# Kernel tuning notes

Hardware: AMD Instinct MI355X
Metric: run time of the kernel (lower is better)

The kernel has to match this reference:

```python
import jax, jax.numpy as jnp
import numpy as np

B, L, H, D = 2, 2048, 16, 64


def setup_inputs() -> dict:
    key = jax.random.key(0)
    k1, k2, k3, k4 = jax.random.split(key, 4)
    query_states = jax.random.normal(k1, (B, L, H, D), dtype=jnp.float32)
    key_states = jax.random.normal(k2, (B, L, H, D), dtype=jnp.float32)
    # per-head linear feature maps (LinearFeatureMap parameters)
    Wq = jax.random.normal(k3, (H, D, D), dtype=jnp.float32)
    Wk = jax.random.normal(k4, (H, D, D), dtype=jnp.float32)
    return {"query_states": query_states, "key_states": key_states, "Wq": Wq, "Wk": Wk}


def reference(query_states, key_states, Wq, Wk):
    # per-head linear feature map: [B,L,H,D] x [H,D,E] -> [B,L,H,E]
    q = jnp.einsum('blhd,hde->blhe', query_states, Wq)
    k = jnp.einsum('blhd,hde->blhe', key_states, Wk)
    # kernelized attention scores: [B,H,L,S]
    attn = jnp.einsum('blhd,bshd->bhls', q, k)
    # sum-normalization over keys (non-softmax normalizer)
    attn = attn / jnp.sum(attn, axis=-1, keepdims=True)
    return attn
```

## Files before the change

kernel.cpp:

```cpp
#include <hip/hip_runtime.h>
#include <stdint.h>

#define NB 2
#define NL 2048
#define NH 16
#define ND 64

typedef __attribute__((ext_vector_type(8))) short short8;
typedef __attribute__((ext_vector_type(4))) float f32x4;
typedef __attribute__((ext_vector_type(4))) unsigned short ushort4v;

__device__ __forceinline__ unsigned short f2bf_rne(float x) {
    union { float f; unsigned int u; } v; v.f = x;
    unsigned int r = v.u + 0x7fffu + ((v.u >> 16) & 1u);
    return (unsigned short)(r >> 16);
}
__device__ __forceinline__ float bf2f(unsigned short b) {
    union { unsigned int u; float f; } v; v.u = ((unsigned int)b) << 16;
    return v.f;
}

__global__ __launch_bounds__(256) void proj_bf16_kernel(const float* __restrict__ x,
                                                        const float* __restrict__ W,
                                                        unsigned short* __restrict__ ph,
                                                        unsigned short* __restrict__ pl) {
    __shared__ float Wlds[ND * ND];
    __shared__ float xs[128 * 68];
    const int blk = blockIdx.x;
    const int lc = blk & 15;
    const int h = (blk >> 4) & 15;
    const int b = blk >> 8;
    const int l0 = lc * 128;
    const int t = threadIdx.x;

    {
        const float4* src = (const float4*)(W + (size_t)h * ND * ND);
#pragma unroll
        for (int i = 0; i < 4; ++i)
            ((float4*)Wlds)[t + 256 * i] = src[t + 256 * i];
    }
    {
#pragma unroll
        for (int i = 0; i < 8; ++i) {
            const int idx = t + 256 * i;
            const int r = idx >> 4, c = idx & 15;
            const float4 v = *(const float4*)(x + (((size_t)b * NL + l0 + r) * NH + h) * ND + c * 4);
            *(float4*)&xs[r * 68 + c * 4] = v;
        }
    }
    __syncthreads();

    const int e4 = (t & 15) * 4;
    const int rg = t >> 4;
    float acc[8][4] = {};
    for (int d = 0; d < ND; ++d) {
        const float4 w4 = *(const float4*)&Wlds[d * ND + e4];
#pragma unroll
        for (int it = 0; it < 8; ++it) {
            const float xv = xs[(rg + it * 16) * 68 + d];
            acc[it][0] += xv * w4.x; acc[it][1] += xv * w4.y;
            acc[it][2] += xv * w4.z; acc[it][3] += xv * w4.w;
        }
    }

    unsigned short* phh = ph + ((size_t)(b * NH + h) * NL + l0) * ND;
    unsigned short* pll = pl + ((size_t)(b * NH + h) * NL + l0) * ND;
#pragma unroll
    for (int it = 0; it < 8; ++it) {
        const int r = rg + it * 16;
        const int ep = e4 ^ ((r & 7) << 3);
        ushort4v hv, lv;
#pragma unroll
        for (int j = 0; j < 4; ++j) {
            const unsigned short hb = f2bf_rne(acc[it][j]);
            hv[j] = hb;
            lv[j] = f2bf_rne(acc[it][j] - bf2f(hb));
        }
        *(ushort4v*)&phh[(size_t)r * ND + ep] = hv;
        *(ushort4v*)&pll[(size_t)r * ND + ep] = lv;
    }
}

__global__ __launch_bounds__(1024) void xsum_kernel(const float* __restrict__ key,
                                                    double* __restrict__ xsumk) {
    __shared__ double part[16][64];
    const int bh = blockIdx.x;
    const int b = bh >> 4, h = bh & 15;
    const int t = threadIdx.x;
    const int e = t & 63, c = t >> 6;
    const float* base = key + ((size_t)b * NL * NH + h) * ND + e;
    double acc = 0.0;
    for (int s = c * 128; s < (c + 1) * 128; ++s)
        acc += (double)base[(size_t)s * (NH * ND)];
    part[c][e] = acc;
    __syncthreads();
    if (t < 64) {
        double s2 = 0.0;
#pragma unroll
        for (int c2 = 0; c2 < 16; ++c2) s2 += part[c2][e];
        xsumk[(size_t)bh * ND + e] = s2;
    }
}

__global__ __launch_bounds__(64) void prep_kernel(const double* __restrict__ xsumk,
                                                  const float* __restrict__ Wq,
                                                  const float* __restrict__ Wk,
                                                  double* __restrict__ v) {
    __shared__ double xs[ND], ks[ND];
    const int bh = blockIdx.x;
    const int h = bh & 15;
    const int t = threadIdx.x;
    xs[t] = xsumk[(size_t)bh * ND + t];
    __syncthreads();
    {
        double acc = 0.0;
        const float* wk = Wk + (size_t)h * ND * ND + t;
        for (int d = 0; d < ND; ++d) acc += xs[d] * (double)wk[(size_t)d * ND];
        ks[t] = acc;
    }
    __syncthreads();
    {
        double acc = 0.0;
        const float* wq = Wq + (size_t)h * ND * ND + (size_t)t * ND;
        for (int e = 0; e < ND; ++e) acc += (double)wq[e] * ks[e];
        v[(size_t)bh * ND + t] = acc;
    }
}

__global__ __launch_bounds__(256) void den_kernel(const float* __restrict__ xq,
                                                  const double* __restrict__ v,
                                                  float* __restrict__ invden) {
    __shared__ double vs[ND];
    const int bh = blockIdx.x;
    const int b = bh >> 4, h = bh & 15;
    const int t = threadIdx.x;
    if (t < 64) vs[t] = v[(size_t)bh * ND + t];
    __syncthreads();
    const int l = blockIdx.y * 256 + t;
    const float* xp = xq + (((size_t)b * NL + l) * NH + h) * ND;
    double acc = 0.0;
#pragma unroll 8
    for (int d = 0; d < ND; ++d) acc += (double)xp[d] * vs[d];
    invden[(size_t)bh * NL + l] = (float)(1.0 / acc);
}

__global__ __launch_bounds__(256) void attn_kernel(const unsigned short* __restrict__ qbh,
                                                   const unsigned short* __restrict__ qbl,
                                                   const unsigned short* __restrict__ kbh,
                                                   const unsigned short* __restrict__ kbl,
                                                   const float* __restrict__ invden,
                                                   float* __restrict__ out) {
    __shared__ unsigned short smem[4 * 128 * 64];
    const int bh = blockIdx.z;
    const int l0 = blockIdx.y * 128, s0 = blockIdx.x * 128;
    const int t = threadIdx.x;
    const int w = t >> 6, ln = t & 63;

    {
        const size_t pan = (size_t)bh * NL * ND;
        const unsigned short* srcs[4] = {qbh + pan + (size_t)l0 * ND,
                                         qbl + pan + (size_t)l0 * ND,
                                         kbh + pan + (size_t)s0 * ND,
                                         kbl + pan + (size_t)s0 * ND};
#pragma unroll
        for (int arr = 0; arr < 4; ++arr) {
            const unsigned short* s = srcs[arr] + w * 2048 + ln * 8;
            unsigned short* d = smem + arr * 8192 + w * 2048;
#pragma unroll
            for (int u = 0; u < 4; ++u) {
                __builtin_amdgcn_global_load_lds((const __attribute__((address_space(1))) unsigned int*)(s + u * 512),
                                                 (__attribute__((address_space(3))) unsigned int*)(d + u * 512),
                                                 16, 0, 0);
            }
        }
    }
    __syncthreads();

    const int wr = w >> 1, wc = w & 1;
    const int fr = ln & 15, g = ln >> 4;
    const int swz = (fr & 7) << 4;

    f32x4 acc[4][4];
#pragma unroll
    for (int i = 0; i < 4; ++i)
#pragma unroll
        for (int j = 0; j < 4; ++j) acc[i][j] = (f32x4){0.f, 0.f, 0.f, 0.f};

    const char* sb = (const char*)smem;
#pragma unroll
    for (int kc = 0; kc < 2; ++kc) {
        const int cofs = ((kc << 6) | (g << 4)) ^ swz;
        short8 kh_f[4], kl_f[4], qh_f[4], ql_f[4];
#pragma unroll
        for (int i = 0; i < 4; ++i) {
            const int arow = wr * 64 + i * 16 + fr;
            kh_f[i] = *(const short8*)(sb + 2 * 16384 + arow * 128 + cofs);
            kl_f[i] = *(const short8*)(sb + 3 * 16384 + arow * 128 + cofs);
            const int brow = wc * 64 + i * 16 + fr;
            qh_f[i] = *(const short8*)(sb + 0 * 16384 + brow * 128 + cofs);
            ql_f[i] = *(const short8*)(sb + 1 * 16384 + brow * 128 + cofs);
        }
#pragma unroll
        for (int i = 0; i < 4; ++i)
#pragma unroll
            for (int j = 0; j < 4; ++j) {
                acc[i][j] = __builtin_amdgcn_mfma_f32_16x16x32_bf16(kh_f[i], qh_f[j], acc[i][j], 0, 0, 0);
                acc[i][j] = __builtin_amdgcn_mfma_f32_16x16x32_bf16(kh_f[i], ql_f[j], acc[i][j], 0, 0, 0);
                acc[i][j] = __builtin_amdgcn_mfma_f32_16x16x32_bf16(kl_f[i], qh_f[j], acc[i][j], 0, 0, 0);
            }
    }

    const float* invp = invden + (size_t)bh * NL + l0 + wc * 64 + fr;
#pragma unroll
    for (int j = 0; j < 4; ++j) {
        const float inv = invp[j * 16];
        float* orow = out + ((size_t)bh * NL + l0 + wc * 64 + j * 16 + fr) * NL + s0 + wr * 64 + g * 4;
#pragma unroll
        for (int i = 0; i < 4; ++i) {
            const f32x4 a = acc[i][j];
            float4 vv;
            vv.x = a[0] * inv; vv.y = a[1] * inv; vv.z = a[2] * inv; vv.w = a[3] * inv;
            *(float4*)(orow + i * 16) = vv;
        }
    }
}

extern "C" void kernel_launch(void* const* d_in, const int* in_sizes, int n_in,
                              void* d_out, int out_size, void* d_ws, size_t ws_size,
                              hipStream_t stream) {
    const float* query = (const float*)d_in[0];
    const float* key   = (const float*)d_in[1];
    const float* Wq    = (const float*)d_in[2];
    const float* Wk    = (const float*)d_in[3];
    float* out = (float*)d_out;

    const size_t npan = (size_t)NB * NH * NL * ND;
    char* ws = (char*)d_ws;
    unsigned short* qbh = (unsigned short*)(ws);
    unsigned short* qbl = (unsigned short*)(ws + 1 * npan * 2);
    unsigned short* kbh = (unsigned short*)(ws + 2 * npan * 2);
    unsigned short* kbl = (unsigned short*)(ws + 3 * npan * 2);
    double* xsumk = (double*)(ws + 4 * npan * 2);
    double* v     = (double*)(ws + 4 * npan * 2 + 16384);
    float* invden = (float*)(ws + 4 * npan * 2 + 32768);

    proj_bf16_kernel<<<NB * NH * (NL / 128), 256, 0, stream>>>(query, Wq, qbh, qbl);
    proj_bf16_kernel<<<NB * NH * (NL / 128), 256, 0, stream>>>(key, Wk, kbh, kbl);
    xsum_kernel<<<NB * NH, 1024, 0, stream>>>(key, xsumk);
    prep_kernel<<<NB * NH, 64, 0, stream>>>(xsumk, Wq, Wk, v);
    den_kernel<<<dim3(NB * NH, NL / 256), 256, 0, stream>>>(query, v, invden);
    attn_kernel<<<dim3(NL / 128, NL / 128, NB * NH), 256, 0, stream>>>(qbh, qbl, kbh, kbl, invden, out);
}
```

Measured before the change: 193.1 us.

## Load MFMA fragments directly from global memory and remap blocks across XCDs

The attention kernel stops staging Q/K bf16 hi/lo tiles in LDS and instead loads each short8 fragment straight from global memory, which removes the LDS swizzle and the block barrier. The projection kernel writes unswizzled layouts to match. The grid is flattened to 1D and block IDs are remapped so that consecutive tiles of the same head land on the same XCD for L2 reuse. Output stores become nontemporal to avoid polluting the cache with the large write-once result. Direct global fragment loads may be less coalesced and rely on L2 hits in exchange for zero LDS traffic.

```diff
diff --git a/kernel.cpp b/kernel.cpp
--- a/kernel.cpp
+++ b/kernel.cpp
@@ -68,7 +68,6 @@
 #pragma unroll
     for (int it = 0; it < 8; ++it) {
         const int r = rg + it * 16;
-        const int ep = e4 ^ ((r & 7) << 3);
         ushort4v hv, lv;
 #pragma unroll
         for (int j = 0; j < 4; ++j) {
@@ -76,8 +75,8 @@
             hv[j] = hb;
             lv[j] = f2bf_rne(acc[it][j] - bf2f(hb));
         }
-        *(ushort4v*)&phh[(size_t)r * ND + ep] = hv;
-        *(ushort4v*)&pll[(size_t)r * ND + ep] = lv;
+        *(ushort4v*)&phh[(size_t)r * ND + e4] = hv;
+        *(ushort4v*)&pll[(size_t)r * ND + e4] = lv;
     }
 }
 
@@ -150,35 +149,21 @@
                                                    const unsigned short* __restrict__ kbl,
                                                    const float* __restrict__ invden,
                                                    float* __restrict__ out) {
-    __shared__ unsigned short smem[4 * 128 * 64];
-    const int bh = blockIdx.z;
-    const int l0 = blockIdx.y * 128, s0 = blockIdx.x * 128;
+    const int orig = blockIdx.x;
+    const int wid = (orig & 7) * 1024 + (orig >> 3);
+    const int st = wid & 15, lt = (wid >> 4) & 15, bh = wid >> 8;
+    const int l0 = lt * 128, s0 = st * 128;
+
     const int t = threadIdx.x;
     const int w = t >> 6, ln = t & 63;
-
-    {
-        const size_t pan = (size_t)bh * NL * ND;
-        const unsigned short* srcs[4] = {qbh + pan + (size_t)l0 * ND,
-                                         qbl + pan + (size_t)l0 * ND,
-                                         kbh + pan + (size_t)s0 * ND,
-                                         kbl + pan + (size_t)s0 * ND};
-#pragma unroll
-        for (int arr = 0; arr < 4; ++arr) {
-            const unsigned short* s = srcs[arr] + w * 2048 + ln * 8;
-            unsigned short* d = smem + arr * 8192 + w * 2048;
-#pragma unroll
-            for (int u = 0; u < 4; ++u) {
-                __builtin_amdgcn_global_load_lds((const __attribute__((address_space(1))) unsigned int*)(s + u * 512),
-                                                 (__attribute__((address_space(3))) unsigned int*)(d + u * 512),
-                                                 16, 0, 0);
-            }
-        }
-    }
-    __syncthreads();
-
     const int wr = w >> 1, wc = w & 1;
     const int fr = ln & 15, g = ln >> 4;
-    const int swz = (fr & 7) << 4;
+
+    const size_t pan = (size_t)bh * NL * ND;
+    const unsigned short* qh_p = qbh + pan;
+    const unsigned short* ql_p = qbl + pan;
+    const unsigned short* kh_p = kbh + pan;
+    const unsigned short* kl_p = kbl + pan;
 
     f32x4 acc[4][4];
 #pragma unroll
@@ -186,19 +171,18 @@
 #pragma unroll
         for (int j = 0; j < 4; ++j) acc[i][j] = (f32x4){0.f, 0.f, 0.f, 0.f};
 
-    const char* sb = (const char*)smem;
 #pragma unroll
     for (int kc = 0; kc < 2; ++kc) {
-        const int cofs = ((kc << 6) | (g << 4)) ^ swz;
+        const int col = kc * 32 + g * 8;
         short8 kh_f[4], kl_f[4], qh_f[4], ql_f[4];
 #pragma unroll
         for (int i = 0; i < 4; ++i) {
-            const int arow = wr * 64 + i * 16 + fr;
-            kh_f[i] = *(const short8*)(sb + 2 * 16384 + arow * 128 + cofs);
-            kl_f[i] = *(const short8*)(sb + 3 * 16384 + arow * 128 + cofs);
-            const int brow = wc * 64 + i * 16 + fr;
-            qh_f[i] = *(const short8*)(sb + 0 * 16384 + brow * 128 + cofs);
-            ql_f[i] = *(const short8*)(sb + 1 * 16384 + brow * 128 + cofs);
+            const size_t arow = (size_t)(s0 + wr * 64 + i * 16 + fr) * ND + col;
+            kh_f[i] = *(const short8*)(kh_p + arow);
+            kl_f[i] = *(const short8*)(kl_p + arow);
+            const size_t brow = (size_t)(l0 + wc * 64 + i * 16 + fr) * ND + col;
+            qh_f[i] = *(const short8*)(qh_p + brow);
+            ql_f[i] = *(const short8*)(ql_p + brow);
         }
 #pragma unroll
         for (int i = 0; i < 4; ++i)
@@ -217,10 +201,9 @@
         float* orow = out + ((size_t)bh * NL + l0 + wc * 64 + j * 16 + fr) * NL + s0 + wr * 64 + g * 4;
 #pragma unroll
         for (int i = 0; i < 4; ++i) {
-            const f32x4 a = acc[i][j];
-            float4 vv;
-            vv.x = a[0] * inv; vv.y = a[1] * inv; vv.z = a[2] * inv; vv.w = a[3] * inv;
-            *(float4*)(orow + i * 16) = vv;
+            f32x4 vv = acc[i][j];
+            vv[0] *= inv; vv[1] *= inv; vv[2] *= inv; vv[3] *= inv;
+            __builtin_nontemporal_store(vv, (f32x4*)(orow + i * 16));
         }
     }
 }
@@ -249,5 +232,5 @@
     xsum_kernel<<<NB * NH, 1024, 0, stream>>>(key, xsumk);
     prep_kernel<<<NB * NH, 64, 0, stream>>>(xsumk, Wq, Wk, v);
     den_kernel<<<dim3(NB * NH, NL / 256), 256, 0, stream>>>(query, v, invden);
-    attn_kernel<<<dim3(NL / 128, NL / 128, NB * NH), 256, 0, stream>>>(qbh, qbl, kbh, kbl, invden, out);
-}
+    attn_kernel<<<NL / 128 * (NL / 128) * NB * NH, 256, 0, stream>>>(qbh, qbl, kbh, kbl, invden, out);
+}
```

Result: slower. 212.1 us (+9.9%).

## Split key-sum reduction across more blocks and interleave MFMA with output stores

Applied to the files above, without the earlier changes.

The key column-sum reduction, which ran as one block per (batch, head), now runs as 16 chunked blocks per (batch, head). Their partial sums are combined in the prep kernel, so the sum uses far more CUs. The attention kernel now keeps only K fragments in registers and computes each 16x16 output tile just before storing it, rather than holding a 4x4 accumulator array until the end. This cuts register pressure and lets MFMA work overlap the global stores, at the cost of reloading Q fragments per column group.

```diff
diff --git a/kernel.cpp b/kernel.cpp
--- a/kernel.cpp
+++ b/kernel.cpp
@@ -81,28 +81,28 @@
     }
 }
 
-__global__ __launch_bounds__(1024) void xsum_kernel(const float* __restrict__ key,
-                                                    double* __restrict__ xsumk) {
-    __shared__ double part[16][64];
-    const int bh = blockIdx.x;
+__global__ __launch_bounds__(256) void ksum_part_kernel(const float* __restrict__ key,
+                                                        double* __restrict__ part) {
+    __shared__ double red[4][64];
+    const int blk = blockIdx.x;
+    const int chunk = blk & 15, bh = blk >> 4;
     const int b = bh >> 4, h = bh & 15;
     const int t = threadIdx.x;
-    const int e = t & 63, c = t >> 6;
+    const int e = t & 63, sub = t >> 6;
     const float* base = key + ((size_t)b * NL * NH + h) * ND + e;
     double acc = 0.0;
-    for (int s = c * 128; s < (c + 1) * 128; ++s)
+    const int s0 = chunk * 128 + sub * 32;
+    for (int s = s0; s < s0 + 32; ++s)
         acc += (double)base[(size_t)s * (NH * ND)];
-    part[c][e] = acc;
+    red[sub][e] = acc;
     __syncthreads();
     if (t < 64) {
-        double s2 = 0.0;
-#pragma unroll
-        for (int c2 = 0; c2 < 16; ++c2) s2 += part[c2][e];
-        xsumk[(size_t)bh * ND + e] = s2;
-    }
-}
-
-__global__ __launch_bounds__(64) void prep_kernel(const double* __restrict__ xsumk,
+        const double s2 = red[0][t] + red[1][t] + red[2][t] + red[3][t];
+        part[(size_t)blk * 64 + t] = s2;
+    }
+}
+
+__global__ __launch_bounds__(64) void prep_kernel(const double* __restrict__ part,
                                                   const float* __restrict__ Wq,
                                                   const float* __restrict__ Wk,
                                                   double* __restrict__ v) {
@@ -110,7 +110,12 @@
     const int bh = blockIdx.x;
     const int h = bh & 15;
     const int t = threadIdx.x;
-    xs[t] = xsumk[(size_t)bh * ND + t];
+    {
+        double a = 0.0;
+#pragma unroll
+        for (int c = 0; c < 16; ++c) a += part[((size_t)bh * 16 + c) * 64 + t];
+        xs[t] = a;
+    }
     __syncthreads();
     {
         double acc = 0.0;
@@ -179,48 +184,44 @@
     const int wr = w >> 1, wc = w & 1;
     const int fr = ln & 15, g = ln >> 4;
     const int swz = (fr & 7) << 4;
-
-    f32x4 acc[4][4];
+    const char* sb = (const char*)smem;
+
+    short8 kh_f[4][2], kl_f[4][2];
 #pragma unroll
     for (int i = 0; i < 4; ++i)
 #pragma unroll
-        for (int j = 0; j < 4; ++j) acc[i][j] = (f32x4){0.f, 0.f, 0.f, 0.f};
-
-    const char* sb = (const char*)smem;
-#pragma unroll
-    for (int kc = 0; kc < 2; ++kc) {
-        const int cofs = ((kc << 6) | (g << 4)) ^ swz;
-        short8 kh_f[4], kl_f[4], qh_f[4], ql_f[4];
-#pragma unroll
-        for (int i = 0; i < 4; ++i) {
+        for (int kc = 0; kc < 2; ++kc) {
+            const int cofs = ((kc << 6) | (g << 4)) ^ swz;
             const int arow = wr * 64 + i * 16 + fr;
-            kh_f[i] = *(const short8*)(sb + 2 * 16384 + arow * 128 + cofs);
-            kl_f[i] = *(const short8*)(sb + 3 * 16384 + arow * 128 + cofs);
-            const int brow = wc * 64 + i * 16 + fr;
-            qh_f[i] = *(const short8*)(sb + 0 * 16384 + brow * 128 + cofs);
-            ql_f[i] = *(const short8*)(sb + 1 * 16384 + brow * 128 + cofs);
-        }
-#pragma unroll
-        for (int i = 0; i < 4; ++i)
-#pragma unroll
-            for (int j = 0; j < 4; ++j) {
-                acc[i][j] = __builtin_amdgcn_mfma_f32_16x16x32_bf16(kh_f[i], qh_f[j], acc[i][j], 0, 0, 0);
-                acc[i][j] = __builtin_amdgcn_mfma_f32_16x16x32_bf16(kh_f[i], ql_f[j], acc[i][j], 0, 0, 0);
-                acc[i][j] = __builtin_amdgcn_mfma_f32_16x16x32_bf16(kl_f[i], qh_f[j], acc[i][j], 0, 0, 0);
-            }
-    }
+            kh_f[i][kc] = *(const short8*)(sb + 2 * 16384 + arow * 128 + cofs);
+            kl_f[i][kc] = *(const short8*)(sb + 3 * 16384 + arow * 128 + cofs);
+        }
 
     const float* invp = invden + (size_t)bh * NL + l0 + wc * 64 + fr;
 #pragma unroll
     for (int j = 0; j < 4; ++j) {
+        short8 qh_f[2], ql_f[2];
+#pragma unroll
+        for (int kc = 0; kc < 2; ++kc) {
+            const int cofs = ((kc << 6) | (g << 4)) ^ swz;
+            const int brow = wc * 64 + j * 16 + fr;
+            qh_f[kc] = *(const short8*)(sb + 0 * 16384 + brow * 128 + cofs);
+            ql_f[kc] = *(const short8*)(sb + 1 * 16384 + brow * 128 + cofs);
+        }
         const float inv = invp[j * 16];
         float* orow = out + ((size_t)bh * NL + l0 + wc * 64 + j * 16 + fr) * NL + s0 + wr * 64 + g * 4;
 #pragma unroll
         for (int i = 0; i < 4; ++i) {
-            const f32x4 a = acc[i][j];
-            float4 vv;
-            vv.x = a[0] * inv; vv.y = a[1] * inv; vv.z = a[2] * inv; vv.w = a[3] * inv;
-            *(float4*)(orow + i * 16) = vv;
+            f32x4 a = (f32x4){0.f, 0.f, 0.f, 0.f};
+#pragma unroll
+            for (int kc = 0; kc < 2; ++kc) {
+                a = __builtin_amdgcn_mfma_f32_16x16x32_bf16(kh_f[i][kc], qh_f[kc], a, 0, 0, 0);
+                a = __builtin_amdgcn_mfma_f32_16x16x32_bf16(kh_f[i][kc], ql_f[kc], a, 0, 0, 0);
+                a = __builtin_amdgcn_mfma_f32_16x16x32_bf16(kl_f[i][kc], qh_f[kc], a, 0, 0, 0);
+            }
+            f32x4 vv = a;
+            vv[0] *= inv; vv[1] *= inv; vv[2] *= inv; vv[3] *= inv;
+            *(f32x4*)(orow + i * 16) = vv;
         }
     }
 }
@@ -240,14 +241,14 @@
     unsigned short* qbl = (unsigned short*)(ws + 1 * npan * 2);
     unsigned short* kbh = (unsigned short*)(ws + 2 * npan * 2);
     unsigned short* kbl = (unsigned short*)(ws + 3 * npan * 2);
-    double* xsumk = (double*)(ws + 4 * npan * 2);
-    double* v     = (double*)(ws + 4 * npan * 2 + 16384);
-    float* invden = (float*)(ws + 4 * npan * 2 + 32768);
+    double* part  = (double*)(ws + 4 * npan * 2);
+    double* v     = (double*)(ws + 4 * npan * 2 + 262144);
+    float* invden = (float*)(ws + 4 * npan * 2 + 262144 + 16384);
 
     proj_bf16_kernel<<<NB * NH * (NL / 128), 256, 0, stream>>>(query, Wq, qbh, qbl);
     proj_bf16_kernel<<<NB * NH * (NL / 128), 256, 0, stream>>>(key, Wk, kbh, kbl);
-    xsum_kernel<<<NB * NH, 1024, 0, stream>>>(key, xsumk);
-    prep_kernel<<<NB * NH, 64, 0, stream>>>(xsumk, Wq, Wk, v);
+    ksum_part_kernel<<<NB * NH * 16, 256, 0, stream>>>(key, part);
+    prep_kernel<<<NB * NH, 64, 0, stream>>>(part, Wq, Wk, v);
     den_kernel<<<dim3(NB * NH, NL / 256), 256, 0, stream>>>(query, v, invden);
     attn_kernel<<<dim3(NL / 128, NL / 128, NB * NH), 256, 0, stream>>>(qbh, qbl, kbh, kbl, invden, out);
 }
```

After: 190.4 us. No clear change (-1.4%).
